# Kernel tuning notes

Hardware: AMD Instinct MI355X
Metric: run time of the kernel (lower is better)

The kernel has to match this reference:

```python
import jax, jax.numpy as jnp
import numpy as np

RADIUS = 1.1
RESOLUTION = 64


def setup_inputs() -> dict:
    key = jax.random.key(0)
    k_x, k_v = jax.random.split(key)
    B, N, D, T = 16, 2048, 3, 64
    x = jax.random.normal(k_x, (B, N, D), dtype=jnp.float32)
    # uniform random directions on the sphere: normalized gaussian columns, shape [D, T]
    v = jax.random.normal(k_v, (D, T), dtype=jnp.float32)
    v = v / jnp.linalg.norm(v, axis=0, keepdims=True)
    lin = jnp.linspace(-RADIUS, RADIUS, RESOLUTION, dtype=jnp.float32)  # [R]
    return {"x": x, "v": v, "lin": lin, "scale": 500}


def reference(x, v, lin, scale):
    # x: [B, N, D], v: [D, T], lin: [R]
    scale = jnp.float32(scale)
    nh = jnp.einsum("bnd,dt->bnt", x, v)  # projected heights [B, N, T]
    # soft-threshold each point against every radius level and accumulate over points
    # diff: [B, R, N, T] -> sum over N -> ECT [B, R, T]
    ect = jnp.sum(jax.nn.sigmoid(scale * (lin[None, :, None, None] - nh[:, None, :, :])), axis=2)
    return ect
```

## Files before the change

### kernel.cpp

```cpp
#include <hip/hip_runtime.h>

#define BB 16
#define NN 2048
#define TT 64
#define RR 64
#define PPT 8
#define NC 8
#define WWIN 28.0f

__device__ inline float load_scale(const void* p) {
    int i = *(const int*)p;
    if (i > 0 && i < (1 << 23)) return (float)i;
    return *(const float*)p;
}

__global__ __launch_bounds__(256, 4)
void ect_kernel(const float* __restrict__ x, const float* __restrict__ v,
                const float* __restrict__ lin, const void* __restrict__ scale_p,
                float* __restrict__ out) {
    __shared__ unsigned s_sig[RR][NC];
    __shared__ unsigned s_cnt[RR][NC];

    const int bt  = blockIdx.x;
    const int b   = bt >> 6;
    const int t   = bt & 63;
    const int tid = threadIdx.x;
    const int c   = tid & (NC - 1);

    ((unsigned*)s_sig)[tid]       = 0u;
    ((unsigned*)s_sig)[tid + 256] = 0u;
    ((unsigned*)s_cnt)[tid]       = 0u;
    ((unsigned*)s_cnt)[tid + 256] = 0u;

    const float K2    = load_scale(scale_p) * 1.44269504088896f;
    const float lo    = -1.1f;
    const float invh  = 63.0f / 2.2f;
    const float hstep = 2.2f / 63.0f;
    const float wnh   = WWIN / K2;
    const float Kh    = K2 * hstep;
    const float dwin  = wnh * invh;
    const float v0 = v[t], v1 = v[TT + t], v2 = v[2 * TT + t];

    __syncthreads();

    const float* xb = x + (size_t)b * NN * 3 + tid * (PPT * 3);
    float4 q[6];
    #pragma unroll
    for (int i = 0; i < 6; ++i) q[i] = ((const float4*)xb)[i];
    const float* xf = (const float*)q;

    #pragma unroll
    for (int p = 0; p < PPT; ++p) {
        float nh = __builtin_fmaf(xf[3*p+0], v0,
                   __builtin_fmaf(xf[3*p+1], v1, xf[3*p+2] * v2));
        float u  = (nh - lo) * invh;
        int r_lo = (int)floorf(u - dwin) + 1;  r_lo = max(r_lo, 0);
        int r_hi = (int)ceilf(u + dwin);       r_hi = max(r_hi, 0);
        int r_end = min(r_hi, RR);

        if (r_hi < RR) atomicAdd(&s_cnt[r_hi][c], 1u);

        float ybase = (nh - lo) * K2;
        #pragma unroll
        for (int j = 0; j < 3; ++j) {
            int r = r_lo + j;
            if (r < r_end) {
                float y  = __builtin_fmaf(-Kh, (float)r, ybase);
                float sg = __builtin_amdgcn_rcpf(1.f + __builtin_amdgcn_exp2f(y));
                unsigned fx = (unsigned)__builtin_fmaf(sg, 1048576.f, 0.5f);
                atomicAdd(&s_sig[r][c], fx);
            }
        }
    }
    __syncthreads();

    if (tid < 64) {
        unsigned sg = 0u, cn = 0u;
        #pragma unroll
        for (int k = 0; k < NC; ++k) { sg += s_sig[tid][k]; cn += s_cnt[tid][k]; }
        #pragma unroll
        for (int d = 1; d < 64; d <<= 1) {
            unsigned up = __shfl_up(cn, d, 64);
            if (tid >= d) cn += up;
        }
        out[((size_t)b * RR + tid) * TT + t] = (float)cn + (float)sg * (1.0f / 1048576.0f);
    }
}

extern "C" void kernel_launch(void* const* d_in, const int* in_sizes, int n_in,
                              void* d_out, int out_size, void* d_ws, size_t ws_size,
                              hipStream_t stream) {
    const float* x    = (const float*)d_in[0];
    const float* v    = (const float*)d_in[1];
    const float* lin  = (const float*)d_in[2];
    const void*  scal = d_in[3];
    float* out = (float*)d_out;

    dim3 grid(BB * TT);
    dim3 block(256);
    ect_kernel<<<grid, block, 0, stream>>>(x, v, lin, scal, out);
}
```

Baseline: 11.02 us.

## Encode sigmoid window as prefix-sum differences with two sigmoids per point

Replaces the separate sigmoid and count shared accumulators with one difference array. Each point now adds three fixed-point deltas (s0, s1-s0, 1-s1) starting at its first active bin, and the existing prefix scan rebuilds the full sigmoid sum. This removes the per-point branchy loop of up to three sigmoids plus a count atomic, leaving two exp/rcp pairs and three unconditional LDS atomics. The cost is a narrower transition window of two evaluated bins, which relies on the sigmoid being steep for the given scale and could lose accuracy at lower scales.

```diff
diff --git a/kernel.cpp b/kernel.cpp
--- a/kernel.cpp
+++ b/kernel.cpp
@@ -4,6 +4,7 @@
 #define NN 2048
 #define TT 64
 #define RR 64
+#define RRD (RR + 3)
 #define PPT 8
 #define NC 8
 #define WWIN 28.0f
@@ -18,8 +19,7 @@
 void ect_kernel(const float* __restrict__ x, const float* __restrict__ v,
                 const float* __restrict__ lin, const void* __restrict__ scale_p,
                 float* __restrict__ out) {
-    __shared__ unsigned s_sig[RR][NC];
-    __shared__ unsigned s_cnt[RR][NC];
+    __shared__ unsigned s_d[RRD][NC];
 
     const int bt  = blockIdx.x;
     const int b   = bt >> 6;
@@ -27,18 +27,15 @@
     const int tid = threadIdx.x;
     const int c   = tid & (NC - 1);
 
-    ((unsigned*)s_sig)[tid]       = 0u;
-    ((unsigned*)s_sig)[tid + 256] = 0u;
-    ((unsigned*)s_cnt)[tid]       = 0u;
-    ((unsigned*)s_cnt)[tid + 256] = 0u;
+    #pragma unroll
+    for (int i = tid; i < RRD * NC; i += 256) ((unsigned*)s_d)[i] = 0u;
 
     const float K2    = load_scale(scale_p) * 1.44269504088896f;
     const float lo    = -1.1f;
     const float invh  = 63.0f / 2.2f;
     const float hstep = 2.2f / 63.0f;
-    const float wnh   = WWIN / K2;
     const float Kh    = K2 * hstep;
-    const float dwin  = wnh * invh;
+    const float dwin  = (WWIN / K2) * invh;
     const float v0 = v[t], v1 = v[TT + t], v2 = v[2 * TT + t];
 
     __syncthreads();
@@ -53,37 +50,34 @@
     for (int p = 0; p < PPT; ++p) {
         float nh = __builtin_fmaf(xf[3*p+0], v0,
                    __builtin_fmaf(xf[3*p+1], v1, xf[3*p+2] * v2));
-        float u  = (nh - lo) * invh;
-        int r_lo = (int)floorf(u - dwin) + 1;  r_lo = max(r_lo, 0);
-        int r_hi = (int)ceilf(u + dwin);       r_hi = max(r_hi, 0);
-        int r_end = min(r_hi, RR);
-
-        if (r_hi < RR) atomicAdd(&s_cnt[r_hi][c], 1u);
-
+        float ub = (nh - lo) * invh;
+        int r0 = (int)floorf(ub - dwin) + 1;
+        r0 = max(r0, 0);
+        r0 = min(r0, RR);
         float ybase = (nh - lo) * K2;
-        #pragma unroll
-        for (int j = 0; j < 3; ++j) {
-            int r = r_lo + j;
-            if (r < r_end) {
-                float y  = __builtin_fmaf(-Kh, (float)r, ybase);
-                float sg = __builtin_amdgcn_rcpf(1.f + __builtin_amdgcn_exp2f(y));
-                unsigned fx = (unsigned)__builtin_fmaf(sg, 1048576.f, 0.5f);
-                atomicAdd(&s_sig[r][c], fx);
-            }
-        }
+        float y0 = __builtin_fmaf(-Kh, (float)r0, ybase);
+        float s0 = __builtin_amdgcn_rcpf(1.f + __builtin_amdgcn_exp2f(y0));
+        float s1 = __builtin_amdgcn_rcpf(1.f + __builtin_amdgcn_exp2f(y0 - Kh));
+        unsigned q0 = (unsigned)__builtin_fmaf(s0,        1048576.f, 0.5f);
+        unsigned q1 = (unsigned)__builtin_fmaf(s1 - s0,   1048576.f, 0.5f);
+        unsigned q2 = (unsigned)__builtin_fmaf(1.f - s1,  1048576.f, 0.5f);
+        unsigned* a = &s_d[r0][c];
+        atomicAdd(a,          q0);
+        atomicAdd(a + NC,     q1);
+        atomicAdd(a + 2*NC,   q2);
     }
     __syncthreads();
 
     if (tid < 64) {
-        unsigned sg = 0u, cn = 0u;
+        unsigned acc = 0u;
         #pragma unroll
-        for (int k = 0; k < NC; ++k) { sg += s_sig[tid][k]; cn += s_cnt[tid][k]; }
+        for (int k = 0; k < NC; ++k) acc += s_d[tid][k];
         #pragma unroll
         for (int d = 1; d < 64; d <<= 1) {
-            unsigned up = __shfl_up(cn, d, 64);
-            if (tid >= d) cn += up;
+            unsigned up = __shfl_up(acc, d, 64);
+            if (tid >= d) acc += up;
         }
-        out[((size_t)b * RR + tid) * TT + t] = (float)cn + (float)sg * (1.0f / 1048576.0f);
+        out[((size_t)b * RR + tid) * TT + t] = (float)acc * (1.0f / 1048576.0f);
     }
 }
 
```

After: 9.999 us. 9.3% less time.
